# Performance work log

Hardware: AMD Instinct MI355X
Metric: run time of the kernel (lower is better)

## Reference

```python
import jax, jax.numpy as jnp
import numpy as np

B, LX, T = 32, 64, 128
D = 512          # d_model
DW = 512         # d_word_vec
V = 32000        # src_vocab_size
AV = 16          # trg_vocab_size (attribute vocab)
YL = 2
LSTM_IN = 2 * DW + 2 * D  # decode_on_y=True


def setup_inputs() -> dict:
    key = jax.random.key(0)
    ks = jax.random.split(key, 20)
    s = 0.02
    attr_tab = jax.random.normal(ks[10], (AV, DW), jnp.float32) * s
    attr_tab = attr_tab.at[0].set(0.0)  # padding_idx=0
    return {
        "x_enc": jax.random.normal(ks[0], (B, LX, 2 * D), jnp.float32),
        "x_enc_k": jax.random.normal(ks[1], (B, LX, D), jnp.float32),
        "dec_h0": jax.random.normal(ks[2], (B, D), jnp.float32),
        "dec_c0": jax.random.normal(ks[3], (B, D), jnp.float32),
        "x_mask": jnp.zeros((B, LX), jnp.bool_),
        "y_train": jax.random.randint(ks[4], (B, YL), 0, AV),
        "x_train": jax.random.randint(ks[5], (B, T), 0, V),
        "word_emb": jax.random.normal(ks[6], (V, DW), jnp.float32) * s,
        "attr_emb_tab": attr_tab,
        "W_ih": jax.random.normal(ks[7], (4 * D, LSTM_IN), jnp.float32) * s,
        "W_hh": jax.random.normal(ks[8], (4 * D, D), jnp.float32) * s,
        "b_ih": jnp.zeros((4 * D,), jnp.float32),
        "b_hh": jnp.zeros((4 * D,), jnp.float32),
        "W_trg": jax.random.normal(ks[9], (D, D), jnp.float32) * s,
        "b_trg": jnp.zeros((D,), jnp.float32),
        "W_att": jax.random.normal(ks[11], (1, D), jnp.float32) * s,
        "b_att": jnp.zeros((1,), jnp.float32),
        "W_cr": jax.random.normal(ks[12], (D, 3 * D), jnp.float32) * s,
        "W_ro": jax.random.normal(ks[13], (V, D), jnp.float32) * s,
    }


def _decode(x_enc, x_enc_k, dec_h0, dec_c0, y_train, x_train, word_emb,
            attr_emb_tab, W_ih, W_hh, b_ih, b_hh, W_trg, b_trg, W_att, b_att,
            W_cr, W_ro):
    x_emb = word_emb[x_train[:, :-1]]          # [B, T-1, DW]
    attr = attr_emb_tab[y_train].sum(axis=1)   # [B, DW]

    def step(carry, x_t):
        h, c, feed = carry
        inp = jnp.concatenate([x_t, attr, feed], axis=1)  # [B, 2DW+2D]
        gates = inp @ W_ih.T + b_ih + h @ W_hh.T + b_hh   # [B, 4D]
        i, f, g, o = jnp.split(gates, 4, axis=1)          # torch order i,f,g,o
        c = jax.nn.sigmoid(f) * c + jax.nn.sigmoid(i) * jnp.tanh(g)
        h = jax.nn.sigmoid(o) * jnp.tanh(c)
        # MlpAttn (attn_mask is ignored in the original)
        q = h @ W_trg.T + b_trg                            # [B, D]
        att_h = jnp.tanh(x_enc_k + q[:, None, :])          # [B, LX, D]
        scores = (att_h @ W_att.T + b_att)[..., 0]         # [B, LX]
        w = jax.nn.softmax(scores, axis=-1)
        ctx = jnp.einsum('bl,bld->bd', w, x_enc)           # [B, 2D]
        pre = jnp.tanh(jnp.concatenate([h, ctx], axis=1) @ W_cr.T)  # [B, D]
        return (h, c, ctx), pre

    feed0 = jnp.zeros((x_enc.shape[0], 2 * D), x_enc.dtype)
    xs = jnp.swapaxes(x_emb, 0, 1)                         # [T-1, B, DW]
    _, pres = jax.lax.scan(step, (dec_h0, dec_c0, feed0), xs)  # [T-1, B, D]
    logits = jnp.einsum('tbd,vd->btv', pres, W_ro)         # [B, T-1, V]
    return logits


def reference(x_enc, x_enc_k, dec_h0, dec_c0, x_mask, y_train, x_train,
              word_emb, attr_emb_tab, W_ih, W_hh, b_ih, b_hh, W_trg, b_trg,
              W_att, b_att, W_cr, W_ro):
    return _decode(x_enc, x_enc_k, dec_h0, dec_c0, y_train, x_train, word_emb,
                   attr_emb_tab, W_ih, W_hh, b_ih, b_hh, W_trg, b_trg, W_att,
                   b_att, W_cr, W_ro)
```

## Files before the change

kernel.cpp:

```cpp
#include <hip/hip_runtime.h>
#include <stdint.h>

typedef unsigned short u16;
using bf16x8 = __attribute__((ext_vector_type(8))) short;
using f32x4  = __attribute__((ext_vector_type(4))) float;

__device__ __forceinline__ float b2f(u16 v) {
  return __uint_as_float(((uint32_t)v) << 16);
}
__device__ __forceinline__ u16 f2b(float f) {
  uint32_t u = __float_as_uint(f);
  u = u + 0x7fffu + ((u >> 16) & 1u);
  return (u16)(u >> 16);
}
__device__ __forceinline__ float ldf(const void* p, size_t i, int f32) {
  return f32 ? ((const float*)p)[i] : b2f(((const u16*)p)[i]);
}
__device__ __forceinline__ float sigf(float x) {
  return __builtin_amdgcn_rcpf(1.f + __expf(-x));
}
__device__ __forceinline__ float tanhf_fast(float x) {
  x = fminf(fmaxf(x, -15.f), 15.f);
  float e = __expf(2.f * x);
  return (e - 1.f) * __builtin_amdgcn_rcpf(e + 1.f);
}

__global__ __launch_bounds__(1024) void k_detect(const u16* __restrict__ x, int* flag) {
  int tid = threadIdx.x;
  u16 v = x[tid];
  int e = (v >> 7) & 0xFF;
  int ok = (e >= 100 && e <= 140) ? 1 : 0;
#pragma unroll
  for (int o = 32; o > 0; o >>= 1) ok += __shfl_down(ok, o);
  __shared__ int s[16];
  if ((tid & 63) == 0) s[tid >> 6] = ok;
  __syncthreads();
  if (tid == 0) {
    int c = 0;
#pragma unroll
    for (int i = 0; i < 16; ++i) c += s[i];
    *flag = (c < 900) ? 1 : 0;
  }
}

__global__ __launch_bounds__(256) void k_conv(u16* __restrict__ dst, const void* __restrict__ src,
                                              int n, const int* __restrict__ flagp) {
  int f32 = *flagp;
  int i = blockIdx.x * 256 + threadIdx.x;
  if (i < n) dst[i] = f32 ? f2b(((const float*)src)[i]) : ((const u16*)src)[i];
}

__global__ __launch_bounds__(256) void k_bias(float* __restrict__ bias, const void* b_ih,
                                              const void* b_hh, const int* __restrict__ flagp) {
  int f32 = *flagp;
  int n = blockIdx.x * 256 + threadIdx.x;
  if (n < 2048) bias[n] = ldf(b_ih, n, f32) + ldf(b_hh, n, f32);
}

template<int EPI>
__global__ __launch_bounds__(256) void gemm_bt(
    const u16* __restrict__ A, int lda,
    const void* __restrict__ B, int ldb,
    int M, int K,
    void* __restrict__ C,
    const float* __restrict__ bias,
    int ldc, const int* __restrict__ flagp)
{
  __shared__ __align__(16) u16 As[128 * 32];
  __shared__ __align__(16) u16 Bs[128 * 32];
  const int f32  = *flagp;
  const int tid  = threadIdx.x;
  const int lane = tid & 63;
  const int wv   = tid >> 6;
  const int wm   = (wv >> 1) * 64;
  const int wn   = (wv & 1) * 64;
  const int n0   = blockIdx.x * 128;
  const int m0   = blockIdx.y * 128;
  const int lr   = lane & 15;
  const int lk   = (lane >> 4) * 8;

  f32x4 acc[4][4] = {};

  for (int k0 = 0; k0 < K; k0 += 32) {
    __syncthreads();
#pragma unroll
    for (int c = 0; c < 2; ++c) {
      int idx = tid + c * 256;
      int row = idx >> 2;
      int col = (idx & 3) * 8;
      int ar = m0 + row; if (ar > M - 1) ar = M - 1;
      *(uint4*)&As[idx * 8] = *(const uint4*)&A[(size_t)ar * lda + k0 + col];
      int br = n0 + row;
      if (f32) {
        const float* bp = (const float*)B + (size_t)br * ldb + k0 + col;
        float4 x0 = *(const float4*)bp;
        float4 x1 = *(const float4*)(bp + 4);
        uint4 pk;
        pk.x = (uint32_t)f2b(x0.x) | ((uint32_t)f2b(x0.y) << 16);
        pk.y = (uint32_t)f2b(x0.z) | ((uint32_t)f2b(x0.w) << 16);
        pk.z = (uint32_t)f2b(x1.x) | ((uint32_t)f2b(x1.y) << 16);
        pk.w = (uint32_t)f2b(x1.z) | ((uint32_t)f2b(x1.w) << 16);
        *(uint4*)&Bs[idx * 8] = pk;
      } else {
        *(uint4*)&Bs[idx * 8] = *(const uint4*)((const u16*)B + (size_t)br * ldb + k0 + col);
      }
    }
    __syncthreads();
    bf16x8 af[4], bfr[4];
#pragma unroll
    for (int i = 0; i < 4; ++i) {
      af[i]  = *(const bf16x8*)&As[(wm + i * 16 + lr) * 32 + lk];
      bfr[i] = *(const bf16x8*)&Bs[(wn + i * 16 + lr) * 32 + lk];
    }
#pragma unroll
    for (int i = 0; i < 4; ++i)
#pragma unroll
      for (int j = 0; j < 4; ++j)
        acc[i][j] = __builtin_amdgcn_mfma_f32_16x16x32_bf16(af[i], bfr[j], acc[i][j], 0, 0, 0);
  }

#pragma unroll
  for (int i = 0; i < 4; ++i) {
#pragma unroll
    for (int j = 0; j < 4; ++j) {
#pragma unroll
      for (int r = 0; r < 4; ++r) {
        int m = m0 + wm + i * 16 + (lane >> 4) * 4 + r;
        int n = n0 + wn + j * 16 + lr;
        if (m < M) {
          float v = acc[i][j][r];
          if (EPI == 0) {
            ((u16*)C)[(size_t)m * ldc + n] = f2b(v + bias[n]);
          } else if (EPI == 1) {
            ((u16*)C)[(size_t)m * ldc + n] = f2b(tanhf_fast(v));
          } else {
            int tt = m >> 5, bb = m & 31;
            size_t off = (size_t)bb * 4064000 + (size_t)tt * 32000 + n;
            if (f32) ((float*)C)[off] = v;
            else     ((u16*)C)[off] = f2b(v);
          }
        }
      }
    }
  }
}

#define NBLK 128
__device__ __forceinline__ void gbar(int* cnt) {
  __syncthreads();
  if (threadIdx.x == 0) {
    __threadfence();
    int t = __hip_atomic_fetch_add(cnt, 1, __ATOMIC_ACQ_REL, __HIP_MEMORY_SCOPE_AGENT);
    int target = (t / NBLK + 1) * NBLK;
    while (__hip_atomic_load(cnt, __ATOMIC_ACQUIRE, __HIP_MEMORY_SCOPE_AGENT) < target) {
      __builtin_amdgcn_s_sleep(1);
    }
    __threadfence();
  }
  __syncthreads();
}

__global__ __launch_bounds__(256, 1) void k_loop(
    const u16* __restrict__ W3,
    const u16* __restrict__ pregates,
    const u16* __restrict__ cxek,
    const u16* __restrict__ cxe,
    const u16* __restrict__ cW_trg,
    const u16* __restrict__ cb_trg,
    const u16* __restrict__ cW_att,
    const float* __restrict__ c_state,
    u16* __restrict__ inpA,
    u16* __restrict__ inpB,
    u16* __restrict__ hctx,
    float* __restrict__ ps,
    int* __restrict__ bar)
{
  const int j   = blockIdx.x;
  const int tid = threadIdx.x;

  __shared__ __align__(16) u16 w3s[16][1544];
  __shared__ __align__(16) u16 wtg[4][520];
  __shared__ __align__(16) u16 xek[32 * 64 * 4];
  __shared__ __align__(16) u16 xes[256 * 64];
  __shared__ __align__(16) u16 hs[32][520];
  __shared__ float gsum[4][32][17];
  __shared__ float qs[128];
  __shared__ float scp[4][64];
  __shared__ float wts[64];
  __shared__ float wa4[4], btg4[4];
  __shared__ float cls[128];

  for (int i = tid; i < 16 * 192; i += 256) {
    int row = i / 192, cc = (i % 192) * 8;
    int gr = (row >> 2) * 512 + j * 4 + (row & 3);
    *(uint4*)&w3s[row][cc] = *(const uint4*)&W3[(size_t)gr * 1536 + cc];
  }
  for (int i = tid; i < 4 * 64; i += 256) {
    int r = i >> 6, cc = (i & 63) * 8;
    *(uint4*)&wtg[r][cc] = *(const uint4*)&cW_trg[((size_t)(j * 4 + r)) * 512 + cc];
  }
  for (int i = tid; i < 2048; i += 256) {
    int b = i >> 6, l = i & 63;
    *(uint2*)&xek[i * 4] = *(const uint2*)&cxek[((size_t)b * 64 + l) * 512 + j * 4];
  }
  for (int i = tid; i < 2048; i += 256) {
    int d = i >> 3, c = i & 7;
    bf16x8 v;
#pragma unroll
    for (int e = 0; e < 8; ++e)
      v[e] = (short)cxe[((size_t)(j >> 2) * 64 + c * 8 + e) * 1024 + (j & 3) * 256 + d];
    *(bf16x8*)&xes[d * 64 + ((c ^ (d & 7)) * 8)] = v;
  }
  if (tid < 4) { wa4[tid] = b2f(cW_att[j * 4 + tid]); btg4[tid] = b2f(cb_trg[j * 4 + tid]); }
  if (tid < 128) cls[tid] = c_state[(tid >> 2) * 512 + j * 4 + (tid & 3)];
  __syncthreads();

  u16* inp  = inpA;
  u16* inpn = inpB;

  for (int t = 0; t < 127; ++t) {
    {
      const int lane = tid & 63, wv = tid >> 6;
      const int lr = lane & 15, lk = (lane >> 4) * 8;
      f32x4 acc0 = {}, acc1 = {};
      const u16* Ar0 = inp + lr * 1536 + wv * 384 + lk;
      const u16* Ar1 = Ar0 + 16 * 1536;
      const u16* Br  = &w3s[lr][wv * 384 + lk];
#pragma unroll 6
      for (int it = 0; it < 12; ++it) {
        bf16x8 a0 = *(const bf16x8*)(Ar0 + it * 32);
        bf16x8 a1 = *(const bf16x8*)(Ar1 + it * 32);
        bf16x8 bb = *(const bf16x8*)(Br + it * 32);
        acc0 = __builtin_amdgcn_mfma_f32_16x16x32_bf16(a0, bb, acc0, 0, 0, 0);
        acc1 = __builtin_amdgcn_mfma_f32_16x16x32_bf16(a1, bb, acc1, 0, 0, 0);
      }
#pragma unroll
      for (int r = 0; r < 4; ++r) {
        int m = (lane >> 4) * 4 + r;
        gsum[wv][m][lr]      = acc0[r];
        gsum[wv][m + 16][lr] = acc1[r];
      }
    }
    __syncthreads();
    if (tid < 128) {
      const int b = tid >> 2, r = tid & 3;
      float gv[4];
#pragma unroll
      for (int g = 0; g < 4; ++g) {
        int n = g * 4 + r;
        float s = gsum[0][b][n] + gsum[1][b][n] + gsum[2][b][n] + gsum[3][b][n];
        gv[g] = s + b2f(pregates[((size_t)t * 32 + b) * 2048 + g * 512 + j * 4 + r]);
      }
      float cn = sigf(gv[1]) * cls[tid] + sigf(gv[0]) * tanhf_fast(gv[2]);
      float hh = sigf(gv[3]) * tanhf_fast(cn);
      cls[tid] = cn;
      u16 hb = f2b(hh);
      int col = j * 4 + r;
      inpn[b * 1536 + 1024 + col] = hb;
      hctx[((size_t)t * 32 + b) * 1536 + col] = hb;
    }
    gbar(bar);

    for (int i = tid; i < 32 * 64; i += 256) {
      int b = i >> 6, cc = (i & 63) * 8;
      *(uint4*)&hs[b][cc] = *(const uint4*)&inpn[b * 1536 + 1024 + cc];
    }
    __syncthreads();
    {
      const int o = tid >> 1, kh = tid & 1;
      const int b = o >> 2, r = o & 3;
      float acc = 0.f;
      const u16* hr = &hs[b][kh * 256];
      const u16* wr = &wtg[r][kh * 256];
#pragma unroll 8
      for (int k = 0; k < 256; k += 8) {
        bf16x8 hv  = *(const bf16x8*)(hr + k);
        bf16x8 wv8 = *(const bf16x8*)(wr + k);
#pragma unroll
        for (int e = 0; e < 8; ++e) acc += b2f((u16)hv[e]) * b2f((u16)wv8[e]);
      }
      acc += __shfl_xor(acc, 1);
      if (kh == 0) qs[o] = acc + btg4[r];
    }
    __syncthreads();
    {
      const int b = tid >> 3, lg = tid & 7;
      const float q0 = qs[b * 4 + 0], q1 = qs[b * 4 + 1];
      const float q2 = qs[b * 4 + 2], q3 = qs[b * 4 + 3];
      const float w0 = wa4[0], w1 = wa4[1], w2 = wa4[2], w3v = wa4[3];
      float* pdst = ps + ((size_t)b * 128 + j) * 64 + lg * 8;
#pragma unroll
      for (int il = 0; il < 8; ++il) {
        int l = lg * 8 + il;
        const u16* xk = &xek[(b * 64 + l) * 4];
        float s = w0 * tanhf_fast(b2f(xk[0]) + q0) + w1 * tanhf_fast(b2f(xk[1]) + q1)
                + w2 * tanhf_fast(b2f(xk[2]) + q2) + w3v * tanhf_fast(b2f(xk[3]) + q3);
        pdst[il] = s;
      }
    }
    gbar(bar);

    {
      const int cb = j >> 2, dq = j & 3;
      {
        const int l = tid & 63, part = tid >> 6;
        const float* pp = ps + ((size_t)cb * 128 + part * 32) * 64 + l;
        float s = 0.f;
#pragma unroll 8
        for (int jj = 0; jj < 32; ++jj) s += pp[jj * 64];
        scp[part][l] = s;
      }
      __syncthreads();
      if (tid < 64) {
        float s = scp[0][tid] + scp[1][tid] + scp[2][tid] + scp[3][tid];
        float mx = s;
#pragma unroll
        for (int o = 32; o > 0; o >>= 1) mx = fmaxf(mx, __shfl_xor(mx, o));
        float e = __expf(s - mx);
        float sm = e;
#pragma unroll
        for (int o = 32; o > 0; o >>= 1) sm += __shfl_xor(sm, o);
        wts[tid] = e * __builtin_amdgcn_rcpf(sm);
      }
      __syncthreads();
      {
        float acc = 0.f;
        const int dsw = tid & 7;
#pragma unroll
        for (int c = 0; c < 8; ++c) {
          bf16x8 v = *(const bf16x8*)&xes[tid * 64 + ((c ^ dsw) * 8)];
#pragma unroll
          for (int e = 0; e < 8; ++e) acc += wts[c * 8 + e] * b2f((u16)v[e]);
        }
        u16 cv = f2b(acc);
        int col = dq * 256 + tid;
        inpn[cb * 1536 + col] = cv;
        hctx[((size_t)t * 32 + cb) * 1536 + 512 + col] = cv;
      }
    }
    gbar(bar);

    u16* tmp = inp; inp = inpn; inpn = tmp;
  }
}

__global__ __launch_bounds__(256) void k_gather(
    const int* __restrict__ x_train, const int* __restrict__ y_train,
    const void* __restrict__ word_emb, const void* __restrict__ attr_tab,
    u16* __restrict__ A_x, const int* __restrict__ flagp)
{
  int f32 = *flagp;
  int idx = blockIdx.x * 256 + threadIdx.x;
  if (idx >= 4064 * 1024) return;
  int m = idx >> 10, k = idx & 1023;
  int t = m >> 5, b = m & 31;
  u16 v;
  if (k < 512) {
    v = f2b(ldf(word_emb, (size_t)x_train[b * 128 + t] * 512 + k, f32));
  } else {
    int d = k - 512;
    float a = ldf(attr_tab, (size_t)y_train[b * 2] * 512 + d, f32) +
              ldf(attr_tab, (size_t)y_train[b * 2 + 1] * 512 + d, f32);
    v = f2b(a);
  }
  A_x[idx] = v;
}

__global__ __launch_bounds__(256) void k_w3(
    const void* __restrict__ W_ih, const void* __restrict__ W_hh,
    u16* __restrict__ W3, const int* __restrict__ flagp)
{
  int f32 = *flagp;
  int idx = blockIdx.x * 256 + threadIdx.x;
  if (idx >= 2048 * 1536) return;
  int n = idx / 1536, k = idx - n * 1536;
  float v = (k < 1024) ? ldf(W_ih, (size_t)n * 2048 + 1024 + k, f32)
                       : ldf(W_hh, (size_t)n * 512 + (k - 1024), f32);
  W3[idx] = f2b(v);
}

__global__ __launch_bounds__(256) void k_init(
    const void* __restrict__ dec_h0, const void* __restrict__ dec_c0,
    u16* __restrict__ inpA, float* __restrict__ c_state,
    int* __restrict__ bar, const int* __restrict__ flagp)
{
  int f32 = *flagp;
  int idx = blockIdx.x * 256 + threadIdx.x;
  if (idx < 32 * 1536) {
    int m = idx / 1536, c = idx - m * 1536;
    inpA[idx] = (c < 1024) ? (u16)0 : f2b(ldf(dec_h0, m * 512 + (c - 1024), f32));
  }
  if (idx < 32 * 512) c_state[idx] = ldf(dec_c0, idx, f32);
  if (idx < 8) bar[idx] = 0;
}

extern "C" void kernel_launch(void* const* d_in, const int* in_sizes, int n_in,
                              void* d_out, int out_size, void* d_ws, size_t ws_size,
                              hipStream_t stream)
{
  const void* x_enc    = d_in[0];
  const void* x_enc_k  = d_in[1];
  const void* dec_h0   = d_in[2];
  const void* dec_c0   = d_in[3];
  const int* y_train   = (const int*)d_in[5];
  const int* x_train   = (const int*)d_in[6];
  const void* word_emb = d_in[7];
  const void* attr_tab = d_in[8];
  const void* W_ih     = d_in[9];
  const void* W_hh     = d_in[10];
  const void* b_ih     = d_in[11];
  const void* b_hh     = d_in[12];
  const void* W_trg    = d_in[13];
  const void* b_trg    = d_in[14];
  const void* W_att    = d_in[15];
  const void* b_att    = d_in[16];
  const void* W_cr     = d_in[17];
  const void* W_ro     = d_in[18];
  (void)b_att;

  char* ws = (char*)d_ws;
  size_t off = 0;
  auto alloc = [&](size_t bytes) -> void* {
    void* p = ws + off;
    off += (bytes + 255) & ~(size_t)255;
    return p;
  };
  u16*   A_x      = (u16*)  alloc(4064ull * 1024 * 2);
  u16*   pregates = (u16*)  alloc(4064ull * 2048 * 2);
  u16*   W3       = (u16*)  alloc(2048ull * 1536 * 2);
  u16*   hctx     = (u16*)  alloc(4064ull * 1536 * 2);
  u16*   pre_all  = (u16*)  alloc(4064ull * 512 * 2);
  u16*   cxe      = (u16*)  alloc(32ull * 64 * 1024 * 2);
  u16*   cxek     = (u16*)  alloc(32ull * 64 * 512 * 2);
  u16*   cW_trg   = (u16*)  alloc(512ull * 512 * 2);
  u16*   cb_trg   = (u16*)  alloc(512 * 2);
  u16*   cW_att   = (u16*)  alloc(512 * 2);
  float* bias     = (float*)alloc(2048 * 4);
  u16*   inpA     = (u16*)  alloc(32 * 1536 * 2);
  u16*   inpB     = (u16*)  alloc(32 * 1536 * 2);
  float* c_state  = (float*)alloc(32 * 512 * 4);
  float* ps_buf   = (float*)alloc(32ull * 128 * 64 * 4);
  int*   bar      = (int*)  alloc(256);
  int*   flag     = (int*)  alloc(256);

  k_detect<<<1, 1024, 0, stream>>>((const u16*)x_enc, flag);

  k_conv<<<(2097152 + 255) / 256, 256, 0, stream>>>(cxe, x_enc, 2097152, flag);
  k_conv<<<(1048576 + 255) / 256, 256, 0, stream>>>(cxek, x_enc_k, 1048576, flag);
  k_conv<<<(262144 + 255) / 256, 256, 0, stream>>>(cW_trg, W_trg, 262144, flag);
  k_conv<<<2, 256, 0, stream>>>(cb_trg, b_trg, 512, flag);
  k_conv<<<2, 256, 0, stream>>>(cW_att, W_att, 512, flag);
  k_bias<<<8, 256, 0, stream>>>(bias, b_ih, b_hh, flag);

  k_init<<<192, 256, 0, stream>>>(dec_h0, dec_c0, inpA, c_state, bar, flag);
  k_gather<<<(4064 * 1024 + 255) / 256, 256, 0, stream>>>(x_train, y_train, word_emb, attr_tab, A_x, flag);
  k_w3<<<(2048 * 1536 + 255) / 256, 256, 0, stream>>>(W_ih, W_hh, W3, flag);

  gemm_bt<0><<<dim3(16, 32), 256, 0, stream>>>(
      A_x, 1024, W_ih, 2048, 4064, 1024, pregates, bias, 2048, flag);

  k_loop<<<NBLK, 256, 0, stream>>>(W3, pregates, cxek, cxe, cW_trg, cb_trg, cW_att,
                                   c_state, inpA, inpB, hctx, ps_buf, bar);

  gemm_bt<1><<<dim3(4, 32), 256, 0, stream>>>(
      hctx, 1536, W_cr, 1536, 4064, 1536, pre_all, nullptr, 512, flag);
  gemm_bt<2><<<dim3(250, 32), 256, 0, stream>>>(
      pre_all, 512, W_ro, 512, 4064, 512, d_out, nullptr, 32000, flag);
}
```

Measured before the change: 6.549 ms.

## Replace atomic-counter grid barrier with flag-array gather/release barrier

The persistent recurrent kernel's grid barrier moves from a single contended atomic counter to per-block arrive flags. These are polled by one wave in block 0, which then writes per-block release flags on separate cache lines. The per-step pregate loads are also issued before the MFMA gate computation so their latency is hidden. The aim is to cut the barrier latency that dominates the 127-step serial loop. The trade-off is an extra hop through block 0 and more barrier memory to initialise.

```diff
diff --git a/kernel.cpp b/kernel.cpp
--- a/kernel.cpp
+++ b/kernel.cpp
@@ -146,15 +146,28 @@
 }
 
 #define NBLK 128
-__device__ __forceinline__ void gbar(int* cnt) {
+__device__ __forceinline__ void gbar2(int* __restrict__ arr, int* __restrict__ rel,
+                                      int seq, int j, int tid) {
   __syncthreads();
-  if (threadIdx.x == 0) {
+  if (tid == 0) {
     __threadfence();
-    int t = __hip_atomic_fetch_add(cnt, 1, __ATOMIC_ACQ_REL, __HIP_MEMORY_SCOPE_AGENT);
-    int target = (t / NBLK + 1) * NBLK;
-    while (__hip_atomic_load(cnt, __ATOMIC_ACQUIRE, __HIP_MEMORY_SCOPE_AGENT) < target) {
+    __hip_atomic_store(&arr[j * 32], seq, __ATOMIC_RELEASE, __HIP_MEMORY_SCOPE_AGENT);
+  }
+  if (blockIdx.x == 0 && tid < 64) {
+    const int i0 = tid, i1 = tid + 64;
+    bool d0 = false, d1 = false;
+    while (true) {
+      if (!d0) d0 = __hip_atomic_load(&arr[i0 * 32], __ATOMIC_ACQUIRE, __HIP_MEMORY_SCOPE_AGENT) >= seq;
+      if (!d1) d1 = __hip_atomic_load(&arr[i1 * 32], __ATOMIC_ACQUIRE, __HIP_MEMORY_SCOPE_AGENT) >= seq;
+      if (__all(d0 && d1)) break;
       __builtin_amdgcn_s_sleep(1);
     }
+    __hip_atomic_store(&rel[i0 * 32], seq, __ATOMIC_RELEASE, __HIP_MEMORY_SCOPE_AGENT);
+    __hip_atomic_store(&rel[i1 * 32], seq, __ATOMIC_RELEASE, __HIP_MEMORY_SCOPE_AGENT);
+  }
+  if (tid == 0) {
+    while (__hip_atomic_load(&rel[j * 32], __ATOMIC_ACQUIRE, __HIP_MEMORY_SCOPE_AGENT) < seq)
+      __builtin_amdgcn_s_sleep(1);
     __threadfence();
   }
   __syncthreads();
@@ -177,6 +190,9 @@
 {
   const int j   = blockIdx.x;
   const int tid = threadIdx.x;
+  int* arr = bar;
+  int* rel = bar + 4096;
+  int seq = 0;
 
   __shared__ __align__(16) u16 w3s[16][1544];
   __shared__ __align__(16) u16 wtg[4][520];
@@ -219,6 +235,15 @@
   u16* inpn = inpB;
 
   for (int t = 0; t < 127; ++t) {
+    float gpre[4];
+    if (tid < 128) {
+      const int b = tid >> 2, r = tid & 3;
+      const u16* pg = pregates + ((size_t)t * 32 + b) * 2048 + j * 4 + r;
+      gpre[0] = b2f(pg[0]);
+      gpre[1] = b2f(pg[512]);
+      gpre[2] = b2f(pg[1024]);
+      gpre[3] = b2f(pg[1536]);
+    }
     {
       const int lane = tid & 63, wv = tid >> 6;
       const int lr = lane & 15, lk = (lane >> 4) * 8;
@@ -249,7 +274,7 @@
       for (int g = 0; g < 4; ++g) {
         int n = g * 4 + r;
         float s = gsum[0][b][n] + gsum[1][b][n] + gsum[2][b][n] + gsum[3][b][n];
-        gv[g] = s + b2f(pregates[((size_t)t * 32 + b) * 2048 + g * 512 + j * 4 + r]);
+        gv[g] = s + gpre[g];
       }
       float cn = sigf(gv[1]) * cls[tid] + sigf(gv[0]) * tanhf_fast(gv[2]);
       float hh = sigf(gv[3]) * tanhf_fast(cn);
@@ -259,7 +284,7 @@
       inpn[b * 1536 + 1024 + col] = hb;
       hctx[((size_t)t * 32 + b) * 1536 + col] = hb;
     }
-    gbar(bar);
+    ++seq; gbar2(arr, rel, seq, j, tid);
 
     for (int i = tid; i < 32 * 64; i += 256) {
       int b = i >> 6, cc = (i & 63) * 8;
@@ -298,7 +323,7 @@
         pdst[il] = s;
       }
     }
-    gbar(bar);
+    ++seq; gbar2(arr, rel, seq, j, tid);
 
     {
       const int cb = j >> 2, dq = j & 3;
@@ -338,7 +363,7 @@
         hctx[((size_t)t * 32 + cb) * 1536 + 512 + col] = cv;
       }
     }
-    gbar(bar);
+    ++seq; gbar2(arr, rel, seq, j, tid);
 
     u16* tmp = inp; inp = inpn; inpn = tmp;
   }
@@ -391,7 +416,7 @@
     inpA[idx] = (c < 1024) ? (u16)0 : f2b(ldf(dec_h0, m * 512 + (c - 1024), f32));
   }
   if (idx < 32 * 512) c_state[idx] = ldf(dec_c0, idx, f32);
-  if (idx < 8) bar[idx] = 0;
+  if (idx < 8192) bar[idx] = 0;
 }
 
 extern "C" void kernel_launch(void* const* d_in, const int* in_sizes, int n_in,
@@ -440,7 +465,7 @@
   u16*   inpB     = (u16*)  alloc(32 * 1536 * 2);
   float* c_state  = (float*)alloc(32 * 512 * 4);
   float* ps_buf   = (float*)alloc(32ull * 128 * 64 * 4);
-  int*   bar      = (int*)  alloc(256);
+  int*   bar      = (int*)  alloc(8192 * 4);
   int*   flag     = (int*)  alloc(256);
 
   k_detect<<<1, 1024, 0, stream>>>((const u16*)x_enc, flag);
```

Result: slower. 7.928 ms (+21.1%).
